# Kernel tuning notes

Hardware: AMD Instinct MI355X
Metric: run time of the kernel (lower is better)

Reference implementation:

```python
import jax, jax.numpy as jnp
import numpy as np

B, S, D_IN, D_OUT = 4, 2048, 1024, 1024


def setup_inputs() -> dict:
    key = jax.random.key(0)
    ks = jax.random.split(key, 7)
    s_in = 1.0 / np.sqrt(D_IN)
    return {
        "x": jax.random.normal(ks[0], (B, S, D_IN), dtype=jnp.float32),
        "Wq": jax.random.uniform(ks[1], (D_IN, D_OUT), jnp.float32, -s_in, s_in),
        "bq": jax.random.uniform(ks[2], (D_OUT,), jnp.float32, -s_in, s_in),
        "Wk": jax.random.uniform(ks[3], (D_IN, D_OUT), jnp.float32, -s_in, s_in),
        "bk": jax.random.uniform(ks[4], (D_OUT,), jnp.float32, -s_in, s_in),
        "Wv": jax.random.uniform(ks[5], (D_IN, D_OUT), jnp.float32, -s_in, s_in),
        "bv": jax.random.uniform(ks[6], (D_OUT,), jnp.float32, -s_in, s_in),
    }


def reference(x, Wq, bq, Wk, bk, Wv, bv):
    # Linear projections (torch Linear: x @ W^T + b; here W stored as [in,out])
    q = x @ Wq + bq  # [B,S,D]
    k = x @ Wk + bk
    v = x @ Wv + bv
    scores = jnp.einsum("bqd,bkd->bqk", q, k)  # [B,S,S]
    # causal mask: positions j > i masked with -inf (applied BEFORE scaling,
    # which is equivalent since -inf/sqrt(d) == -inf)
    seq = scores.shape[-1]
    causal = jnp.tril(jnp.ones((seq, seq), dtype=bool))
    masked = jnp.where(causal, scores, -jnp.inf)
    attn = jax.nn.softmax(masked / np.sqrt(k.shape[-1]), axis=-1)
    # dropout p=0.0 -> identity
    return attn @ v  # [B,S,D]
```

## Files before the change

kernel.cpp:

```cpp
#include <hip/hip_runtime.h>

typedef unsigned short u16;
typedef unsigned int u32;
typedef __attribute__((ext_vector_type(8))) short short8;
typedef __attribute__((ext_vector_type(4))) float f32x4;

__device__ __forceinline__ u16 f2bf(float f) {
    u32 u = __float_as_uint(f);
    u32 r = (u + 0x7fffu + ((u >> 16) & 1u)) >> 16;
    return (u16)r;
}
__device__ __forceinline__ float bf2f(u16 h) {
    return __uint_as_float(((u32)h) << 16);
}

__device__ __forceinline__ void gld16(u16* lds_dst, const u16* g_src) {
    __builtin_amdgcn_global_load_lds(
        (const __attribute__((address_space(1))) unsigned int*)g_src,
        (__attribute__((address_space(3))) unsigned int*)lds_dst,
        16, 0, 0);
}

__global__ void split_x_k(const float* __restrict__ x, u16* __restrict__ xh,
                          u16* __restrict__ xl) {
    long i = ((long)blockIdx.x * 256 + threadIdx.x) * 4;
    float4 f = *(const float4*)(x + i);
    u16 h0 = f2bf(f.x), h1 = f2bf(f.y), h2 = f2bf(f.z), h3 = f2bf(f.w);
    u16 l0 = f2bf(f.x - bf2f(h0)), l1 = f2bf(f.y - bf2f(h1));
    u16 l2 = f2bf(f.z - bf2f(h2)), l3 = f2bf(f.w - bf2f(h3));
    uint2 hv, lv;
    hv.x = (u32)h0 | ((u32)h1 << 16); hv.y = (u32)h2 | ((u32)h3 << 16);
    lv.x = (u32)l0 | ((u32)l1 << 16); lv.y = (u32)l2 | ((u32)l3 << 16);
    *(uint2*)(xh + i) = hv;
    *(uint2*)(xl + i) = lv;
}

__global__ void splitT_w_k(const float* __restrict__ Wq, const float* __restrict__ Wk,
                           const float* __restrict__ Wv, u16* __restrict__ wth,
                           u16* __restrict__ wtl) {
    __shared__ float tile[32][33];
    int z = blockIdx.z;
    const float* W = (z == 0) ? Wq : (z == 1) ? Wk : Wv;
    int n0 = blockIdx.x * 32, k0 = blockIdx.y * 32;
    int tx = threadIdx.x, ty = threadIdx.y;
#pragma unroll
    for (int r0 = 0; r0 < 4; ++r0) {
        int r = ty + r0 * 8;
        tile[r][tx] = W[(long)(k0 + r) * 1024 + n0 + tx];
    }
    __syncthreads();
    long zoff = (long)z * 1024 * 1024;
#pragma unroll
    for (int r0 = 0; r0 < 4; ++r0) {
        int r = ty + r0 * 8;
        float f = tile[tx][r];
        u16 h = f2bf(f), l = f2bf(f - bf2f(h));
        long idx = zoff + (long)(n0 + r) * 1024 + k0 + tx;
        wth[idx] = h;
        wtl[idx] = l;
    }
}

__global__ void transpose_v_k(const u16* __restrict__ vh, const u16* __restrict__ vl,
                              u16* __restrict__ vth, u16* __restrict__ vtl) {
    __shared__ u16 th[32][33];
    __shared__ u16 tl[32][33];
    int z = blockIdx.z;
    int d0 = blockIdx.x * 32, s0 = blockIdx.y * 32;
    int tx = threadIdx.x, ty = threadIdx.y;
#pragma unroll
    for (int r0 = 0; r0 < 4; ++r0) {
        int r = ty + r0 * 8;
        long idx = ((long)z * 2048 + s0 + r) * 1024 + d0 + tx;
        th[r][tx] = vh[idx];
        tl[r][tx] = vl[idx];
    }
    __syncthreads();
    long zoff = (long)z * 1024 * 2048;
#pragma unroll
    for (int r0 = 0; r0 < 4; ++r0) {
        int r = ty + r0 * 8;
        long idx = zoff + (long)(d0 + r) * 2048 + s0 + tx;
        vth[idx] = th[tx][r];
        vtl[idx] = tl[tx][r];
    }
}

__launch_bounds__(512, 2)
__global__ void gemm_k(const u16* __restrict__ Ah, const u16* __restrict__ Al,
                       const u16* __restrict__ Bh, const u16* __restrict__ Bl,
                       u16* __restrict__ oh0, u16* __restrict__ oh1, u16* __restrict__ oh2,
                       u16* __restrict__ ol0, u16* __restrict__ ol1, u16* __restrict__ ol2,
                       const float* __restrict__ b0, const float* __restrict__ b1,
                       const float* __restrict__ b2) {
    constexpr int NF = 4;
    constexpr int BN = 256;
    constexpr int SLOT = 8192 + NF * 4096;
    __shared__ u16 lds[3 * SLOT];

    const int bi = blockIdx.x, bj = blockIdx.y, z = blockIdx.z;
    const int nsteps = 32;

    const u16* gA_h = Ah;
    const u16* gA_l = Al;
    const u16* gB_h = Bh + (long)z * 1024 * 1024;
    const u16* gB_l = Bl + (long)z * 1024 * 1024;

    const int tid = threadIdx.x;
    const int lane = tid & 63, w = tid >> 6;
    const int wr = w >> 2, wc = w & 3;

    const int srow = tid >> 2;
    const int ls8 = (((tid & 3) ^ ((tid >> 3) & 3)) << 3);
    const long aoff  = ((long)bi * 128 + srow) * 1024 + ls8;
    const long boff0 = ((long)bj * BN + srow) * 1024 + ls8;
    const long boff1 = boff0 + 128L * 1024;
    const int wbase = w * 512;

    f32x4 acc[4][NF] = {};

    const int fr = lane & 15;
    const int ps8 = (((lane >> 4) ^ ((fr >> 1) & 3)) << 3);

    auto stage = [&](int slot, int step) {
        const int k0 = step * 32;
        u16* sb = lds + slot * SLOT;
        gld16(sb + wbase,               gA_h + aoff + k0);
        gld16(sb + 4096 + wbase,        gA_l + aoff + k0);
        gld16(sb + 8192 + wbase,        gB_h + boff0 + k0);
        gld16(sb + 12288 + wbase,       gB_h + boff1 + k0);
        gld16(sb + 16384 + wbase,       gB_l + boff0 + k0);
        gld16(sb + 20480 + wbase,       gB_l + boff1 + k0);
    };

    auto compute = [&](int slot) {
        const u16* LA = lds + slot * SLOT;
        const u16* LB = LA + 8192;
        short8 afh[4], afl[4], bfh[NF], bfl[NF];
#pragma unroll
        for (int m = 0; m < 4; ++m) {
            int off = (wr * 64 + m * 16 + fr) * 32 + ps8;
            afh[m] = *(const short8*)(LA + off);
            afl[m] = *(const short8*)(LA + 4096 + off);
        }
#pragma unroll
        for (int n = 0; n < NF; ++n) {
            int off = (wc * (NF * 16) + n * 16 + fr) * 32 + ps8;
            bfh[n] = *(const short8*)(LB + off);
            bfl[n] = *(const short8*)(LB + NF * 2048 + off);
        }
        __builtin_amdgcn_s_setprio(1);
#pragma unroll
        for (int m = 0; m < 4; ++m)
#pragma unroll
            for (int n = 0; n < NF; ++n) {
                acc[m][n] = __builtin_amdgcn_mfma_f32_16x16x32_bf16(afh[m], bfh[n], acc[m][n], 0, 0, 0);
                acc[m][n] = __builtin_amdgcn_mfma_f32_16x16x32_bf16(afh[m], bfl[n], acc[m][n], 0, 0, 0);
                acc[m][n] = __builtin_amdgcn_mfma_f32_16x16x32_bf16(afl[m], bfh[n], acc[m][n], 0, 0, 0);
            }
        __builtin_amdgcn_s_setprio(0);
    };

    stage(0, 0);
    stage(1, 1);
    int cs = 0, ns = 2;
    for (int h = 0; h < nsteps; ++h) {
        if (h + 1 < nsteps) {
            asm volatile("s_waitcnt vmcnt(6)" ::: "memory");
        } else {
            asm volatile("s_waitcnt vmcnt(0)" ::: "memory");
        }
        __builtin_amdgcn_s_barrier();
        __builtin_amdgcn_sched_barrier(0);
        if (h + 2 < nsteps) stage(ns, h + 2);
        compute(cs);
        cs = (cs == 2) ? 0 : cs + 1;
        ns = (ns == 2) ? 0 : ns + 1;
    }

    const int row0 = bi * 128 + wr * 64 + (lane >> 4) * 4;
    const int col0 = bj * BN + wc * (NF * 16) + (lane & 15);

    const float* bias = (z == 0) ? b0 : (z == 1) ? b1 : b2;
    u16* oh = (z == 0) ? oh0 : (z == 1) ? oh1 : oh2;
    u16* ol = (z == 0) ? ol0 : (z == 1) ? ol1 : ol2;
#pragma unroll
    for (int n = 0; n < NF; ++n) {
        float bv = bias[col0 + n * 16];
#pragma unroll
        for (int m = 0; m < 4; ++m)
#pragma unroll
            for (int j = 0; j < 4; ++j) {
                float v = acc[m][n][j] + bv;
                long idx = (long)(row0 + m * 16 + j) * 1024 + col0 + n * 16;
                u16 h = f2bf(v);
                oh[idx] = h;
                ol[idx] = f2bf(v - bf2f(h));
            }
    }
}

__launch_bounds__(512, 2)
__global__ void qk_k(const u16* __restrict__ Qh, const u16* __restrict__ Ql,
                     const u16* __restrict__ Kh, const u16* __restrict__ Kl,
                     float* __restrict__ S) {
    constexpr int SLOT = 16384;
    __shared__ u16 lds[2 * SLOT];

    const int orig = blockIdx.y * 16 + blockIdx.x;
    const int swz = (orig & 7) * 32 + (orig >> 3);
    const int bi = swz & 15, bj = swz >> 4, z = blockIdx.z;
    if (bj > bi) return;
    const int nsteps = 32;

    const u16* gA_h = Qh + (long)z * 2048 * 1024;
    const u16* gA_l = Ql + (long)z * 2048 * 1024;
    const u16* gB_h = Kh + (long)z * 2048 * 1024;
    const u16* gB_l = Kl + (long)z * 2048 * 1024;

    const int tid = threadIdx.x;
    const int lane = tid & 63, w = tid >> 6;
    const int wr = w >> 2, wc = w & 3;

    const int srow = tid >> 2;
    const int ls8 = (((tid & 3) ^ ((tid >> 3) & 3)) << 3);
    const long aoff  = ((long)bi * 128 + srow) * 1024 + ls8;
    const long boff0 = ((long)bj * 128 + srow) * 1024 + ls8;
    const int wbase = w * 512;

    f32x4 acc[4][2] = {};
    const int fr = lane & 15;
    const int ps8 = (((lane >> 4) ^ ((fr >> 1) & 3)) << 3);

    auto stage = [&](int slot, int step) {
        const int k0 = step * 32;
        u16* sb = lds + slot * SLOT;
        gld16(sb + wbase,         gA_h + aoff + k0);
        gld16(sb + 4096 + wbase,  gA_l + aoff + k0);
        gld16(sb + 8192 + wbase,  gB_h + boff0 + k0);
        gld16(sb + 12288 + wbase, gB_l + boff0 + k0);
    };

    auto compute = [&](int slot) {
        const u16* LA = lds + slot * SLOT;
        const u16* LB = LA + 8192;
        short8 afh[4], afl[4], bfh[2], bfl[2];
#pragma unroll
        for (int m = 0; m < 4; ++m) {
            int off = (wr * 64 + m * 16 + fr) * 32 + ps8;
            afh[m] = *(const short8*)(LA + off);
            afl[m] = *(const short8*)(LA + 4096 + off);
        }
#pragma unroll
        for (int n = 0; n < 2; ++n) {
            int off = (wc * 32 + n * 16 + fr) * 32 + ps8;
            bfh[n] = *(const short8*)(LB + off);
            bfl[n] = *(const short8*)(LB + 4096 + off);
        }
        __builtin_amdgcn_s_setprio(1);
#pragma unroll
        for (int m = 0; m < 4; ++m)
#pragma unroll
            for (int n = 0; n < 2; ++n) {
                acc[m][n] = __builtin_amdgcn_mfma_f32_16x16x32_bf16(afh[m], bfh[n], acc[m][n], 0, 0, 0);
                acc[m][n] = __builtin_amdgcn_mfma_f32_16x16x32_bf16(afh[m], bfl[n], acc[m][n], 0, 0, 0);
                acc[m][n] = __builtin_amdgcn_mfma_f32_16x16x32_bf16(afl[m], bfh[n], acc[m][n], 0, 0, 0);
            }
        __builtin_amdgcn_s_setprio(0);
    };

    stage(0, 0);
    int cs = 0;
    for (int h = 0; h < nsteps; ++h) {
        asm volatile("s_waitcnt vmcnt(0)" ::: "memory");
        __builtin_amdgcn_s_barrier();
        __builtin_amdgcn_sched_barrier(0);
        if (h + 1 < nsteps) stage(cs ^ 1, h + 1);
        compute(cs);
        cs ^= 1;
    }

    const int row0 = bi * 128 + wr * 64 + (lane >> 4) * 4;
    const int col0 = bj * 128 + wc * 32 + (lane & 15);
    float* o = S + (long)z * 2048 * 2048;
#pragma unroll
    for (int m = 0; m < 4; ++m)
#pragma unroll
        for (int n = 0; n < 2; ++n)
#pragma unroll
            for (int j = 0; j < 4; ++j)
                o[(long)(row0 + m * 16 + j) * 2048 + col0 + n * 16] = acc[m][n][j];
}

__global__ void rowred_k(const float* __restrict__ S, float2* __restrict__ stats) {
    const long row = blockIdx.x;
    const int i = (int)(row & 2047);
    const float* srow = S + row * 2048;
    const int t = threadIdx.x;

    float v[8];
    float m = -1e30f;
#pragma unroll
    for (int j = 0; j < 8; ++j) {
        int c = j * 256 + t;
        float x = (c <= i) ? srow[c] : -1e30f;
        v[j] = x;
        m = fmaxf(m, x);
    }
#pragma unroll
    for (int off = 32; off; off >>= 1) m = fmaxf(m, __shfl_xor(m, off));
    __shared__ float redm[4], reds[4];
    if ((t & 63) == 0) redm[t >> 6] = m;
    __syncthreads();
    m = fmaxf(fmaxf(redm[0], redm[1]), fmaxf(redm[2], redm[3]));

    float s = 0.f;
#pragma unroll
    for (int j = 0; j < 8; ++j) {
        int c = j * 256 + t;
        float e = (c <= i) ? __expf((v[j] - m) * 0.03125f) : 0.f;
        s += e;
    }
#pragma unroll
    for (int off = 32; off; off >>= 1) s += __shfl_xor(s, off);
    if ((t & 63) == 0) reds[t >> 6] = s;
    __syncthreads();
    s = reds[0] + reds[1] + reds[2] + reds[3];
    if (t == 0) stats[row] = make_float2(m, 1.f / s);
}

__launch_bounds__(512, 2)
__global__ void pv_k(const float* __restrict__ S, const float2* __restrict__ stats,
                     const u16* __restrict__ Vth, const u16* __restrict__ Vtl,
                     float* __restrict__ out) {
    constexpr int SLOT = 16384;
    __shared__ u16 lds[2 * SLOT];

    const int bi = 15 - (int)blockIdx.x;
    const int bj = blockIdx.y, z = blockIdx.z;
    const int nsteps = (bi + 1) * 4;

    const float* gS = S + (long)z * 2048 * 2048;
    const float2* gst = stats + (long)z * 2048;
    const u16* gB_h = Vth + (long)z * 1024 * 2048;
    const u16* gB_l = Vtl + (long)z * 1024 * 2048;

    const int tid = threadIdx.x;
    const int lane = tid & 63, w = tid >> 6;
    const int wr = w >> 2, wc = w & 3;

    const int srow = tid >> 2;
    const int ls8 = (((tid & 3) ^ ((tid >> 3) & 3)) << 3);
    const int arow = bi * 128 + srow;
    const long arowoff = (long)arow * 2048;
    const long boff0 = ((long)bj * 128 + srow) * 2048 + ls8;
    const int wbase = w * 512;

    const float2 st = gst[arow];
    const float mrow = st.x, inv = st.y;

    f32x4 acc[4][2] = {};
    const int fr = lane & 15;
    const int ps8 = (((lane >> 4) ^ ((fr >> 1) & 3)) << 3);

    float4 sv0, sv1;

    auto loadS = [&](int step) {
        const float* p = gS + arowoff + step * 32 + ls8;
        sv0 = *(const float4*)p;
        sv1 = *(const float4*)(p + 4);
    };
    auto stageV = [&](int slot, int step) {
        u16* sb = lds + slot * SLOT;
        gld16(sb + 8192 + wbase,  gB_h + boff0 + step * 32);
        gld16(sb + 12288 + wbase, gB_l + boff0 + step * 32);
    };
    auto writeP = [&](int slot, int step) {
        const int c0 = step * 32 + ls8;
        float sf[8] = {sv0.x, sv0.y, sv0.z, sv0.w, sv1.x, sv1.y, sv1.z, sv1.w};
        u16 h8[8], l8[8];
#pragma unroll
        for (int e = 0; e < 8; ++e) {
            float p = ((c0 + e) <= arow) ? __expf((sf[e] - mrow) * 0.03125f) * inv : 0.f;
            u16 h = f2bf(p);
            h8[e] = h;
            l8[e] = f2bf(p - bf2f(h));
        }
        u16* sb = lds + slot * SLOT;
        *(short8*)(sb + wbase + lane * 8)        = *(const short8*)h8;
        *(short8*)(sb + 4096 + wbase + lane * 8) = *(const short8*)l8;
    };
    auto compute = [&](int slot) {
        const u16* LA = lds + slot * SLOT;
        const u16* LB = LA + 8192;
        short8 afh[4], afl[4], bfh[2], bfl[2];
#pragma unroll
        for (int m = 0; m < 4; ++m) {
            int off = (wr * 64 + m * 16 + fr) * 32 + ps8;
            afh[m] = *(const short8*)(LA + off);
            afl[m] = *(const short8*)(LA + 4096 + off);
        }
#pragma unroll
        for (int n = 0; n < 2; ++n) {
            int off = (wc * 32 + n * 16 + fr) * 32 + ps8;
            bfh[n] = *(const short8*)(LB + off);
            bfl[n] = *(const short8*)(LB + 4096 + off);
        }
        __builtin_amdgcn_s_setprio(1);
#pragma unroll
        for (int m = 0; m < 4; ++m)
#pragma unroll
            for (int n = 0; n < 2; ++n) {
                acc[m][n] = __builtin_amdgcn_mfma_f32_16x16x32_bf16(afh[m], bfh[n], acc[m][n], 0, 0, 0);
                acc[m][n] = __builtin_amdgcn_mfma_f32_16x16x32_bf16(afh[m], bfl[n], acc[m][n], 0, 0, 0);
                acc[m][n] = __builtin_amdgcn_mfma_f32_16x16x32_bf16(afl[m], bfh[n], acc[m][n], 0, 0, 0);
            }
        __builtin_amdgcn_s_setprio(0);
    };

    loadS(0);
    stageV(0, 0);
    asm volatile("s_waitcnt vmcnt(0)" ::: "memory");
    writeP(0, 0);
    asm volatile("s_waitcnt lgkmcnt(0)" ::: "memory");
    __builtin_amdgcn_s_barrier();
    __builtin_amdgcn_sched_barrier(0);

    int cs = 0;
    for (int h = 0; h < nsteps; ++h) {
        if (h + 1 < nsteps) { loadS(h + 1); stageV(cs ^ 1, h + 1); }
        compute(cs);
        if (h + 1 < nsteps) {
            asm volatile("s_waitcnt vmcnt(0)" ::: "memory");
            writeP(cs ^ 1, h + 1);
            asm volatile("s_waitcnt lgkmcnt(0)" ::: "memory");
        }
        __builtin_amdgcn_s_barrier();
        __builtin_amdgcn_sched_barrier(0);
        cs ^= 1;
    }

    const int row0 = bi * 128 + wr * 64 + (lane >> 4) * 4;
    const int col0 = bj * 128 + wc * 32 + (lane & 15);
    float* o = out + (long)z * 2048 * 1024;
#pragma unroll
    for (int m = 0; m < 4; ++m)
#pragma unroll
        for (int n = 0; n < 2; ++n)
#pragma unroll
            for (int j = 0; j < 4; ++j)
                o[(long)(row0 + m * 16 + j) * 1024 + col0 + n * 16] = acc[m][n][j];
}

extern "C" void kernel_launch(void* const* d_in, const int* in_sizes, int n_in,
                              void* d_out, int out_size, void* d_ws, size_t ws_size,
                              hipStream_t stream) {
    const float* x  = (const float*)d_in[0];
    const float* Wq = (const float*)d_in[1];
    const float* bq = (const float*)d_in[2];
    const float* Wk = (const float*)d_in[3];
    const float* bk = (const float*)d_in[4];
    const float* Wv = (const float*)d_in[5];
    const float* bv = (const float*)d_in[6];
    float* out = (float*)d_out;
    char* ws = (char*)d_ws;
    const size_t MB = 1ull << 20;

    u16* xs_hi = (u16*)(ws + 0 * MB);
    u16* xs_lo = (u16*)(ws + 16 * MB);
    u16* wt_hi = (u16*)(ws + 32 * MB);
    u16* wt_lo = (u16*)(ws + 38 * MB);
    float* S   = (float*)(ws + 0 * MB);
    u16* q_hi = (u16*)(ws + 64 * MB);
    u16* q_lo = (u16*)(ws + 80 * MB);
    u16* k_hi = (u16*)(ws + 96 * MB);
    u16* k_lo = (u16*)(ws + 112 * MB);
    float2* stats = (float2*)(ws + 64 * MB);
    u16* v_hi  = (u16*)(ws + 128 * MB);
    u16* v_lo  = (u16*)(ws + 144 * MB);
    u16* vt_hi = (u16*)(ws + 160 * MB);
    u16* vt_lo = (u16*)(ws + 176 * MB);

    split_x_k<<<8192, 256, 0, stream>>>(x, xs_hi, xs_lo);
    splitT_w_k<<<dim3(32, 32, 3), dim3(32, 8), 0, stream>>>(Wq, Wk, Wv, wt_hi, wt_lo);
    gemm_k<<<dim3(64, 4, 3), 512, 0, stream>>>(
        xs_hi, xs_lo, wt_hi, wt_lo, q_hi, k_hi, v_hi, q_lo, k_lo, v_lo, bq, bk, bv);
    transpose_v_k<<<dim3(32, 64, 4), dim3(32, 8), 0, stream>>>(v_hi, v_lo, vt_hi, vt_lo);
    qk_k<<<dim3(16, 16, 4), 512, 0, stream>>>(q_hi, q_lo, k_hi, k_lo, S);
    rowred_k<<<8192, 256, 0, stream>>>(S, stats);
    pv_k<<<dim3(16, 8, 4), 512, 0, stream>>>(S, stats, vt_hi, vt_lo, out);
}
```

Baseline: 488.6 us.

## Materialize normalized split-bf16 P in softmax and stream it into PV via LDS

The row-reduction kernel now also computes the normalized probabilities and writes them as bf16 hi/lo pairs, up to the causal 128-column tile limit. The PV kernel drops its in-loop exp, normalize and split work and instead stages P tiles asynchronously into LDS, the same way it stages V, with a simpler double-buffered loop. This takes VALU exp/convert work and register-to-LDS writes off the MFMA pipeline, at the cost of an extra write and read of P through global memory. It also splits the fused QKV projection into three launches and removes the QK block-index swizzle, which may hurt cache locality or add launch overhead.

```diff
diff --git a/kernel.cpp b/kernel.cpp
--- a/kernel.cpp
+++ b/kernel.cpp
@@ -87,24 +87,17 @@
 }
 
 __launch_bounds__(512, 2)
-__global__ void gemm_k(const u16* __restrict__ Ah, const u16* __restrict__ Al,
+__global__ void proj_k(const u16* __restrict__ Ah, const u16* __restrict__ Al,
                        const u16* __restrict__ Bh, const u16* __restrict__ Bl,
-                       u16* __restrict__ oh0, u16* __restrict__ oh1, u16* __restrict__ oh2,
-                       u16* __restrict__ ol0, u16* __restrict__ ol1, u16* __restrict__ ol2,
-                       const float* __restrict__ b0, const float* __restrict__ b1,
-                       const float* __restrict__ b2) {
+                       u16* __restrict__ oh, u16* __restrict__ ol,
+                       const float* __restrict__ bias) {
     constexpr int NF = 4;
     constexpr int BN = 256;
     constexpr int SLOT = 8192 + NF * 4096;
     __shared__ u16 lds[3 * SLOT];
 
-    const int bi = blockIdx.x, bj = blockIdx.y, z = blockIdx.z;
+    const int bi = blockIdx.x, bj = blockIdx.y;
     const int nsteps = 32;
-
-    const u16* gA_h = Ah;
-    const u16* gA_l = Al;
-    const u16* gB_h = Bh + (long)z * 1024 * 1024;
-    const u16* gB_l = Bl + (long)z * 1024 * 1024;
 
     const int tid = threadIdx.x;
     const int lane = tid & 63, w = tid >> 6;
@@ -125,12 +118,12 @@
     auto stage = [&](int slot, int step) {
         const int k0 = step * 32;
         u16* sb = lds + slot * SLOT;
-        gld16(sb + wbase,               gA_h + aoff + k0);
-        gld16(sb + 4096 + wbase,        gA_l + aoff + k0);
-        gld16(sb + 8192 + wbase,        gB_h + boff0 + k0);
-        gld16(sb + 12288 + wbase,       gB_h + boff1 + k0);
-        gld16(sb + 16384 + wbase,       gB_l + boff0 + k0);
-        gld16(sb + 20480 + wbase,       gB_l + boff1 + k0);
+        gld16(sb + wbase,               Ah + aoff + k0);
+        gld16(sb + 4096 + wbase,        Al + aoff + k0);
+        gld16(sb + 8192 + wbase,        Bh + boff0 + k0);
+        gld16(sb + 12288 + wbase,       Bh + boff1 + k0);
+        gld16(sb + 16384 + wbase,       Bl + boff0 + k0);
+        gld16(sb + 20480 + wbase,       Bl + boff1 + k0);
     };
 
     auto compute = [&](int slot) {
@@ -180,10 +173,6 @@
 
     const int row0 = bi * 128 + wr * 64 + (lane >> 4) * 4;
     const int col0 = bj * BN + wc * (NF * 16) + (lane & 15);
-
-    const float* bias = (z == 0) ? b0 : (z == 1) ? b1 : b2;
-    u16* oh = (z == 0) ? oh0 : (z == 1) ? oh1 : oh2;
-    u16* ol = (z == 0) ? ol0 : (z == 1) ? ol1 : ol2;
 #pragma unroll
     for (int n = 0; n < NF; ++n) {
         float bv = bias[col0 + n * 16];
@@ -207,9 +196,7 @@
     constexpr int SLOT = 16384;
     __shared__ u16 lds[2 * SLOT];
 
-    const int orig = blockIdx.y * 16 + blockIdx.x;
-    const int swz = (orig & 7) * 32 + (orig >> 3);
-    const int bi = swz & 15, bj = swz >> 4, z = blockIdx.z;
+    const int bi = blockIdx.x, bj = blockIdx.y, z = blockIdx.z;
     if (bj > bi) return;
     const int nsteps = 32;
 
@@ -292,11 +279,15 @@
                 o[(long)(row0 + m * 16 + j) * 2048 + col0 + n * 16] = acc[m][n][j];
 }
 
-__global__ void rowred_k(const float* __restrict__ S, float2* __restrict__ stats) {
+__global__ void softmax_k(const float* __restrict__ S, u16* __restrict__ Ph,
+                          u16* __restrict__ Pl) {
     const long row = blockIdx.x;
     const int i = (int)(row & 2047);
     const float* srow = S + row * 2048;
+    u16* ph = Ph + row * 2048;
+    u16* pl = Pl + row * 2048;
     const int t = threadIdx.x;
+    const int limit = ((i >> 7) + 1) << 7;
 
     float v[8];
     float m = -1e30f;
@@ -314,11 +305,13 @@
     __syncthreads();
     m = fmaxf(fmaxf(redm[0], redm[1]), fmaxf(redm[2], redm[3]));
 
+    float p[8];
     float s = 0.f;
 #pragma unroll
     for (int j = 0; j < 8; ++j) {
         int c = j * 256 + t;
         float e = (c <= i) ? __expf((v[j] - m) * 0.03125f) : 0.f;
+        p[j] = e;
         s += e;
     }
 #pragma unroll
@@ -326,11 +319,21 @@
     if ((t & 63) == 0) reds[t >> 6] = s;
     __syncthreads();
     s = reds[0] + reds[1] + reds[2] + reds[3];
-    if (t == 0) stats[row] = make_float2(m, 1.f / s);
+    const float inv = 1.f / s;
+#pragma unroll
+    for (int j = 0; j < 8; ++j) {
+        int c = j * 256 + t;
+        if (c < limit) {
+            float o = p[j] * inv;
+            u16 h = f2bf(o);
+            ph[c] = h;
+            pl[c] = f2bf(o - bf2f(h));
+        }
+    }
 }
 
 __launch_bounds__(512, 2)
-__global__ void pv_k(const float* __restrict__ S, const float2* __restrict__ stats,
+__global__ void pv_k(const u16* __restrict__ Ph, const u16* __restrict__ Pl,
                      const u16* __restrict__ Vth, const u16* __restrict__ Vtl,
                      float* __restrict__ out) {
     constexpr int SLOT = 16384;
@@ -340,8 +343,8 @@
     const int bj = blockIdx.y, z = blockIdx.z;
     const int nsteps = (bi + 1) * 4;
 
-    const float* gS = S + (long)z * 2048 * 2048;
-    const float2* gst = stats + (long)z * 2048;
+    const u16* gA_h = Ph + (long)z * 2048 * 2048;
+    const u16* gA_l = Pl + (long)z * 2048 * 2048;
     const u16* gB_h = Vth + (long)z * 1024 * 2048;
     const u16* gB_l = Vtl + (long)z * 1024 * 2048;
 
@@ -351,45 +354,23 @@
 
     const int srow = tid >> 2;
     const int ls8 = (((tid & 3) ^ ((tid >> 3) & 3)) << 3);
-    const int arow = bi * 128 + srow;
-    const long arowoff = (long)arow * 2048;
+    const long aoff  = ((long)bi * 128 + srow) * 2048 + ls8;
     const long boff0 = ((long)bj * 128 + srow) * 2048 + ls8;
     const int wbase = w * 512;
-
-    const float2 st = gst[arow];
-    const float mrow = st.x, inv = st.y;
 
     f32x4 acc[4][2] = {};
     const int fr = lane & 15;
     const int ps8 = (((lane >> 4) ^ ((fr >> 1) & 3)) << 3);
 
-    float4 sv0, sv1;
-
-    auto loadS = [&](int step) {
-        const float* p = gS + arowoff + step * 32 + ls8;
-        sv0 = *(const float4*)p;
-        sv1 = *(const float4*)(p + 4);
-    };
-    auto stageV = [&](int slot, int step) {
+    auto stage = [&](int slot, int step) {
+        const int k0 = step * 32;
         u16* sb = lds + slot * SLOT;
-        gld16(sb + 8192 + wbase,  gB_h + boff0 + step * 32);
-        gld16(sb + 12288 + wbase, gB_l + boff0 + step * 32);
-    };
-    auto writeP = [&](int slot, int step) {
-        const int c0 = step * 32 + ls8;
-        float sf[8] = {sv0.x, sv0.y, sv0.z, sv0.w, sv1.x, sv1.y, sv1.z, sv1.w};
-        u16 h8[8], l8[8];
-#pragma unroll
-        for (int e = 0; e < 8; ++e) {
-            float p = ((c0 + e) <= arow) ? __expf((sf[e] - mrow) * 0.03125f) * inv : 0.f;
-            u16 h = f2bf(p);
-            h8[e] = h;
-            l8[e] = f2bf(p - bf2f(h));
-        }
-        u16* sb = lds + slot * SLOT;
-        *(short8*)(sb + wbase + lane * 8)        = *(const short8*)h8;
-        *(short8*)(sb + 4096 + wbase + lane * 8) = *(const short8*)l8;
-    };
+        gld16(sb + wbase,         gA_h + aoff + k0);
+        gld16(sb + 4096 + wbase,  gA_l + aoff + k0);
+        gld16(sb + 8192 + wbase,  gB_h + boff0 + k0);
+        gld16(sb + 12288 + wbase, gB_l + boff0 + k0);
+    };
+
     auto compute = [&](int slot) {
         const u16* LA = lds + slot * SLOT;
         const u16* LB = LA + 8192;
@@ -418,25 +399,14 @@
         __builtin_amdgcn_s_setprio(0);
     };
 
-    loadS(0);
-    stageV(0, 0);
-    asm volatile("s_waitcnt vmcnt(0)" ::: "memory");
-    writeP(0, 0);
-    asm volatile("s_waitcnt lgkmcnt(0)" ::: "memory");
-    __builtin_amdgcn_s_barrier();
-    __builtin_amdgcn_sched_barrier(0);
-
+    stage(0, 0);
     int cs = 0;
     for (int h = 0; h < nsteps; ++h) {
-        if (h + 1 < nsteps) { loadS(h + 1); stageV(cs ^ 1, h + 1); }
-        compute(cs);
-        if (h + 1 < nsteps) {
-            asm volatile("s_waitcnt vmcnt(0)" ::: "memory");
-            writeP(cs ^ 1, h + 1);
-            asm volatile("s_waitcnt lgkmcnt(0)" ::: "memory");
-        }
+        asm volatile("s_waitcnt vmcnt(0)" ::: "memory");
         __builtin_amdgcn_s_barrier();
         __builtin_amdgcn_sched_barrier(0);
+        if (h + 1 < nsteps) stage(cs ^ 1, h + 1);
+        compute(cs);
         cs ^= 1;
     }
 
@@ -475,18 +445,22 @@
     u16* q_lo = (u16*)(ws + 80 * MB);
     u16* k_hi = (u16*)(ws + 96 * MB);
     u16* k_lo = (u16*)(ws + 112 * MB);
-    float2* stats = (float2*)(ws + 64 * MB);
+    u16* P_hi = (u16*)(ws + 64 * MB);
+    u16* P_lo = (u16*)(ws + 96 * MB);
     u16* v_hi  = (u16*)(ws + 128 * MB);
     u16* v_lo  = (u16*)(ws + 144 * MB);
     u16* vt_hi = (u16*)(ws + 160 * MB);
     u16* vt_lo = (u16*)(ws + 176 * MB);
 
+    const long WZ = 1024L * 1024;
+
     split_x_k<<<8192, 256, 0, stream>>>(x, xs_hi, xs_lo);
     splitT_w_k<<<dim3(32, 32, 3), dim3(32, 8), 0, stream>>>(Wq, Wk, Wv, wt_hi, wt_lo);
-    gemm_k<<<dim3(64, 4, 3), 512, 0, stream>>>(
-        xs_hi, xs_lo, wt_hi, wt_lo, q_hi, k_hi, v_hi, q_lo, k_lo, v_lo, bq, bk, bv);
+    proj_k<<<dim3(64, 4), 512, 0, stream>>>(xs_hi, xs_lo, wt_hi,          wt_lo,          q_hi, q_lo, bq);
+    proj_k<<<dim3(64, 4), 512, 0, stream>>>(xs_hi, xs_lo, wt_hi + WZ,     wt_lo + WZ,     k_hi, k_lo, bk);
+    proj_k<<<dim3(64, 4), 512, 0, stream>>>(xs_hi, xs_lo, wt_hi + 2 * WZ, wt_lo + 2 * WZ, v_hi, v_lo, bv);
     transpose_v_k<<<dim3(32, 64, 4), dim3(32, 8), 0, stream>>>(v_hi, v_lo, vt_hi, vt_lo);
     qk_k<<<dim3(16, 16, 4), 512, 0, stream>>>(q_hi, q_lo, k_hi, k_lo, S);
-    rowred_k<<<8192, 256, 0, stream>>>(S, stats);
-    pv_k<<<dim3(16, 8, 4), 512, 0, stream>>>(S, stats, vt_hi, vt_lo, out);
-}
+    softmax_k<<<8192, 256, 0, stream>>>(S, P_hi, P_lo);
+    pv_k<<<dim3(16, 8, 4), 512, 0, stream>>>(P_hi, P_lo, vt_hi, vt_lo, out);
+}
```

Result: faster. 460.2 us (-5.8%).
